# Performance work log

Hardware: AMD Instinct MI355X
Metric: run time of the kernel (lower is better)

## Reference

```python
import jax, jax.numpy as jnp
import numpy as np

D_MODEL = 2048
NUM_HEADS = 16
HEAD_DIM = D_MODEL // NUM_HEADS


def setup_inputs() -> dict:
    key = jax.random.key(0)
    ks = jax.random.split(key, 9)
    B, S, D = 2, 2048, D_MODEL
    scale = 1.0 / np.sqrt(D)
    x = jax.random.normal(ks[0], (B, S, D), dtype=jnp.float32)
    # torch nn.Linear weights are [out, in]; y = x @ W.T + b
    wq = jax.random.normal(ks[1], (D, D), dtype=jnp.float32) * scale
    wk = jax.random.normal(ks[2], (D, D), dtype=jnp.float32) * scale
    wv = jax.random.normal(ks[3], (D, D), dtype=jnp.float32) * scale
    wo = jax.random.normal(ks[4], (D, D), dtype=jnp.float32) * scale
    bq = jax.random.normal(ks[5], (D,), dtype=jnp.float32) * scale
    bk = jax.random.normal(ks[6], (D,), dtype=jnp.float32) * scale
    bv = jax.random.normal(ks[7], (D,), dtype=jnp.float32) * scale
    bo = jax.random.normal(ks[8], (D,), dtype=jnp.float32) * scale
    return {"x": x, "wq": wq, "bq": bq, "wk": wk, "bk": bk,
            "wv": wv, "bv": bv, "wo": wo, "bo": bo}


def reference(x, wq, bq, wk, bk, wv, bv, wo, bo):
    B, S, D = x.shape
    H, Dh = NUM_HEADS, HEAD_DIM
    # projections (torch Linear: x @ W.T + b), reshape to [B, H, S, Dh]
    q = (x @ wq.T + bq).reshape(B, S, H, Dh).transpose(0, 2, 1, 3)
    k = (x @ wk.T + bk).reshape(B, S, H, Dh).transpose(0, 2, 1, 3)
    v = (x @ wv.T + bv).reshape(B, S, H, Dh).transpose(0, 2, 1, 3)
    scores = jnp.einsum("bhqd,bhkd->bhqk", q, k) / jnp.sqrt(jnp.float32(Dh))
    attn = jax.nn.softmax(scores, axis=-1)
    out = jnp.einsum("bhqk,bhkd->bhqd", attn, v)  # [B, H, S, Dh]
    out = out.transpose(0, 2, 1, 3).reshape(B, S, D)
    return out @ wo.T + bo
```

## Files before the change

kernel.cpp:

```cpp
#include <hip/hip_runtime.h>

#define DEV __device__ __forceinline__

typedef __attribute__((ext_vector_type(8))) short bf16x8;
typedef __attribute__((ext_vector_type(4))) float f32x4;

constexpr int D_MODEL = 2048;
constexpr int NHEAD = 16;
constexpr int DH = 128;
constexpr int SS = 2048;
constexpr int KK = 2048;

DEV unsigned short f2bf(float f) {
  unsigned int u = __builtin_bit_cast(unsigned int, f);
  u = (u + 0x7fff + ((u >> 16) & 1)) >> 16;
  return (unsigned short)u;
}

DEV void async16(const void* g, void* l) {
  __builtin_amdgcn_global_load_lds(
      (const __attribute__((address_space(1))) unsigned int*)g,
      (__attribute__((address_space(3))) unsigned int*)l, 16, 0, 0);
}

DEV f32x4 mfma16(bf16x8 a, bf16x8 b, f32x4 c) {
  return __builtin_amdgcn_mfma_f32_16x16x32_bf16(a, b, c, 0, 0, 0);
}

__global__ __launch_bounds__(256) void cast_all(
    const float* __restrict__ x, const float* __restrict__ wq,
    const float* __restrict__ wk, const float* __restrict__ wv,
    const float* __restrict__ wo, unsigned short* __restrict__ xb,
    unsigned short* __restrict__ wb) {
  long i4 = ((long)blockIdx.x * 256 + threadIdx.x) * 4;
  const float* src;
  unsigned short* dst;
  long off;
  if (i4 < 8388608) {
    src = x; dst = xb; off = i4;
  } else {
    long j = i4 - 8388608;
    int seg = (int)(j >> 22);
    off = j & 4194303;
    src = (seg == 0) ? wq : (seg == 1) ? wk : (seg == 2) ? wv : wo;
    dst = wb + ((long)seg << 22);
  }
  float4 v = *(const float4*)(src + off);
  ushort4 u;
  u.x = f2bf(v.x); u.y = f2bf(v.y); u.z = f2bf(v.z); u.w = f2bf(v.w);
  *(ushort4*)(dst + off) = u;
}

template <int MODE>
__global__ __launch_bounds__(256, 2) void gemm_bt(
    const unsigned short* __restrict__ A, const unsigned short* __restrict__ W,
    const float* __restrict__ b0, const float* __restrict__ b1,
    const float* __restrict__ b2, unsigned short* __restrict__ oq,
    unsigned short* __restrict__ ok, unsigned short* __restrict__ ov,
    float* __restrict__ of) {
  __shared__ unsigned short lA[128 * 32];
  __shared__ unsigned short lB[128 * 32];
  const int t = threadIdx.x;
  const int lane = t & 63, wid = t >> 6;
  const int m0 = blockIdx.y * 128, n0 = blockIdx.x * 128;
  const int srow = t >> 2, scol = (t & 3) * 8;
  const unsigned short* ga = A + (long)(m0 + srow) * KK + scol;
  const unsigned short* gw = W + (long)(n0 + srow) * KK + scol;
  const int i16 = lane & 15, g4 = lane >> 4;
  const int wr = wid >> 1, wc = wid & 1;
  f32x4 acc[4][4] = {};
  for (int k0 = 0; k0 < KK; k0 += 32) {
    async16(ga + k0, &lA[wid * 512]);
    async16(ga + 64 * KK + k0, &lA[2048 + wid * 512]);
    async16(gw + k0, &lB[wid * 512]);
    async16(gw + 64 * KK + k0, &lB[2048 + wid * 512]);
    __syncthreads();
    bf16x8 af[4], bfr[4];
#pragma unroll
    for (int i = 0; i < 4; i++)
      af[i] = *(const bf16x8*)&lA[(wr * 64 + i * 16 + i16) * 32 + g4 * 8];
#pragma unroll
    for (int j = 0; j < 4; j++)
      bfr[j] = *(const bf16x8*)&lB[(wc * 64 + j * 16 + i16) * 32 + g4 * 8];
#pragma unroll
    for (int i = 0; i < 4; i++)
#pragma unroll
      for (int j = 0; j < 4; j++) acc[i][j] = mfma16(af[i], bfr[j], acc[i][j]);
    __syncthreads();
  }
#pragma unroll
  for (int i = 0; i < 4; i++) {
#pragma unroll
    for (int j = 0; j < 4; j++) {
      const int ng = n0 + wc * 64 + j * 16 + i16;
#pragma unroll
      for (int r = 0; r < 4; r++) {
        const int mg = m0 + wr * 64 + i * 16 + g4 * 4 + r;
        float v = acc[i][j][r];
        if (MODE == 1) {
          v += b0[ng];
          of[(long)mg * D_MODEL + ng] = v;
        } else {
          const int seg = ng >> 11, n = ng & 2047;
          const int h = n >> 7, d = n & 127;
          const int b_ = mg >> 11, s_ = mg & 2047;
          const long bh = b_ * NHEAD + h;
          if (seg == 0) {
            v = (v + b0[n]) * 0.08838834764831845f;
            oq[(bh * SS + s_) * DH + d] = f2bf(v);
          } else if (seg == 1) {
            v += b1[n];
            ok[(bh * SS + s_) * DH + d] = f2bf(v);
          } else {
            v += b2[n];
            ov[(bh * DH + d) * SS + s_] = f2bf(v);
          }
        }
      }
    }
  }
}

__global__ __launch_bounds__(256, 2) void attn_fwd(
    const unsigned short* __restrict__ Q, const unsigned short* __restrict__ Kb,
    const unsigned short* __restrict__ Vt, unsigned short* __restrict__ Ob) {
  __shared__ unsigned short lK[2][64 * 128];
  __shared__ unsigned short lV[2][128 * 64];
  __shared__ unsigned short lP[4][16 * 64];
  const int t = threadIdx.x, lane = t & 63, wid = t >> 6;
  const int i16 = lane & 15, g4 = lane >> 4;
  const int qt = blockIdx.x, bh = blockIdx.y;
  bf16x8 qa[2][4];
#pragma unroll
  for (int qi = 0; qi < 2; qi++) {
    const long qrow = (long)bh * SS + qt * 128 + wid * 32 + qi * 16 + i16;
#pragma unroll
    for (int ks = 0; ks < 4; ks++)
      qa[qi][ks] = *(const bf16x8*)&Q[qrow * DH + ks * 32 + g4 * 8];
  }
  f32x4 o[2][8] = {};
  float mrow[2][4] = {{-1e30f, -1e30f, -1e30f, -1e30f},
                      {-1e30f, -1e30f, -1e30f, -1e30f}};
  float lrow[2][4] = {};
  const char* kbase = (const char*)(Kb + (long)bh * SS * DH);
  const char* vbase = (const char*)(Vt + (long)bh * DH * SS);

  auto STAGE = [&](int buf, int kv0) {
#pragma unroll
    for (int r = 0; r < 4; r++) {
      const int o_ = r * 4096 + t * 16;
      const int okk = o_ ^ (((o_ >> 8) & 7) << 4);
      async16(kbase + (long)kv0 * 256 + okk,
              (char*)lK + buf * 16384 + r * 4096 + wid * 1024);
      const int vrow = o_ >> 7;
      const int inr = (o_ ^ ((vrow & 7) << 4)) & 127;
      async16(vbase + (long)vrow * (SS * 2) + kv0 * 2 + inr,
              (char*)lV + buf * 16384 + r * 4096 + wid * 1024);
    }
  };

  STAGE(0, 0);
  asm volatile("s_waitcnt vmcnt(0)");
  __syncthreads();
  int cur = 0;
  for (int it = 0; it < SS / 64; ++it) {
    if (it + 1 < SS / 64) STAGE(cur ^ 1, (it + 1) * 64);
    const char* kb = (const char*)lK + cur * 16384;
    const char* vb = (const char*)lV + cur * 16384;
    f32x4 s4[2][4] = {};
    __builtin_amdgcn_s_setprio(1);
#pragma unroll
    for (int kc = 0; kc < 4; kc++) {
      const int row = kc * 16 + i16;
#pragma unroll
      for (int ks = 0; ks < 4; ks++) {
        const int lb = row * 256 + ((ks * 64 + g4 * 16) ^ ((row & 7) << 4));
        bf16x8 kf = *(const bf16x8*)(kb + lb);
        s4[0][kc] = mfma16(qa[0][ks], kf, s4[0][kc]);
        s4[1][kc] = mfma16(qa[1][ks], kf, s4[1][kc]);
      }
    }
    __builtin_amdgcn_s_setprio(0);
    float fac[2][4];
#pragma unroll
    for (int qi = 0; qi < 2; qi++) {
#pragma unroll
      for (int r = 0; r < 4; r++) {
        float mx = fmaxf(fmaxf(s4[qi][0][r], s4[qi][1][r]),
                         fmaxf(s4[qi][2][r], s4[qi][3][r]));
        mx = fmaxf(mx, __shfl_xor(mx, 1));
        mx = fmaxf(mx, __shfl_xor(mx, 2));
        mx = fmaxf(mx, __shfl_xor(mx, 4));
        mx = fmaxf(mx, __shfl_xor(mx, 8));
        const float mnew = fmaxf(mrow[qi][r], mx);
        fac[qi][r] = __expf(mrow[qi][r] - mnew);
        mrow[qi][r] = mnew;
#pragma unroll
        for (int kc = 0; kc < 4; kc++)
          s4[qi][kc][r] = __expf(s4[qi][kc][r] - mnew);
        float su = s4[qi][0][r] + s4[qi][1][r] + s4[qi][2][r] + s4[qi][3][r];
        su += __shfl_xor(su, 1);
        su += __shfl_xor(su, 2);
        su += __shfl_xor(su, 4);
        su += __shfl_xor(su, 8);
        lrow[qi][r] = lrow[qi][r] * fac[qi][r] + su;
      }
    }
    bf16x8 pa[2][2];
#pragma unroll
    for (int qi = 0; qi < 2; qi++) {
#pragma unroll
      for (int r = 0; r < 4; r++) {
        const int prow = g4 * 4 + r;
        const int swz = (prow & 7) << 4;
#pragma unroll
        for (int kc = 0; kc < 4; kc++) {
          const int col = kc * 16 + i16;
          *(unsigned short*)((char*)&lP[wid][0] + prow * 128 +
                             ((col * 2) ^ swz)) = f2bf(s4[qi][kc][r]);
        }
      }
#pragma unroll
      for (int ks = 0; ks < 2; ks++) {
        const int lb = i16 * 128 + ((ks * 64 + g4 * 16) ^ ((i16 & 7) << 4));
        pa[qi][ks] = *(const bf16x8*)((const char*)&lP[wid][0] + lb);
      }
    }
#pragma unroll
    for (int qi = 0; qi < 2; qi++)
#pragma unroll
      for (int df = 0; df < 8; df++)
#pragma unroll
        for (int r = 0; r < 4; r++) o[qi][df][r] *= fac[qi][r];
    __builtin_amdgcn_s_setprio(1);
#pragma unroll
    for (int df = 0; df < 8; df++) {
#pragma unroll
      for (int ks = 0; ks < 2; ks++) {
        const int row = df * 16 + i16;
        const int lb = row * 128 + ((ks * 64 + g4 * 16) ^ ((row & 7) << 4));
        bf16x8 vf = *(const bf16x8*)(vb + lb);
        o[0][df] = mfma16(pa[0][ks], vf, o[0][df]);
        o[1][df] = mfma16(pa[1][ks], vf, o[1][df]);
      }
    }
    __builtin_amdgcn_s_setprio(0);
    asm volatile("s_waitcnt vmcnt(0)");
    __syncthreads();
    cur ^= 1;
  }
  const int b_ = bh >> 4, h = bh & 15;
#pragma unroll
  for (int qi = 0; qi < 2; qi++) {
#pragma unroll
    for (int df = 0; df < 8; df++) {
#pragma unroll
      for (int r = 0; r < 4; r++) {
        const float v = o[qi][df][r] / lrow[qi][r];
        const long mg =
            (long)b_ * SS + qt * 128 + wid * 32 + qi * 16 + g4 * 4 + r;
        Ob[mg * D_MODEL + h * DH + df * 16 + i16] = f2bf(v);
      }
    }
  }
}

extern "C" void kernel_launch(void* const* d_in, const int* in_sizes, int n_in,
                              void* d_out, int out_size, void* d_ws,
                              size_t ws_size, hipStream_t stream) {
  const float* x = (const float*)d_in[0];
  const float* wq = (const float*)d_in[1];
  const float* bq = (const float*)d_in[2];
  const float* wk = (const float*)d_in[3];
  const float* bk = (const float*)d_in[4];
  const float* wv = (const float*)d_in[5];
  const float* bv = (const float*)d_in[6];
  const float* wo = (const float*)d_in[7];
  const float* bo = (const float*)d_in[8];
  char* ws = (char*)d_ws;
  unsigned short* xb = (unsigned short*)(ws);
  unsigned short* wb = (unsigned short*)(ws + (16l << 20));
  unsigned short* wob = (unsigned short*)(ws + (40l << 20));
  unsigned short* Qb = (unsigned short*)(ws + (48l << 20));
  unsigned short* Kbf = (unsigned short*)(ws + (64l << 20));
  unsigned short* Vtb = (unsigned short*)(ws + (80l << 20));
  unsigned short* Atb = (unsigned short*)(ws);

  cast_all<<<24576, 256, 0, stream>>>(x, wq, wk, wv, wo, xb, wb);
  gemm_bt<0><<<dim3(48, 32), 256, 0, stream>>>(xb, wb, bq, bk, bv, Qb, Kbf,
                                               Vtb, nullptr);
  attn_fwd<<<dim3(16, 32), 256, 0, stream>>>(Qb, Kbf, Vtb, Atb);
  gemm_bt<1><<<dim3(16, 32), 256, 0, stream>>>(
      Atb, wob, bo, nullptr, nullptr, nullptr, nullptr, nullptr,
      (float*)d_out);
}
```

Measured before the change: 470.4 us.

## Use exp2 softmax with lazy rescaling and MFMA-computed row sums in attention

Folds log2(e) into the Q scaling so the softmax can use the raw v_exp_f32 (exp2) instruction directly. Output rescaling is skipped unless some row's running max grows by more than 8 (in log2 units), checked wave-uniformly with __all. Row sums are computed with an extra MFMA against a vector of bf16 ones instead of shuffle reductions, and the final divide becomes a reciprocal multiply. This removes per-tile shuffles, exps and rescale multiplies. In exchange it allows unnormalized values up to 2^8 and sums the bf16-rounded probabilities, which changes numerics slightly.

```diff
diff --git a/kernel.cpp b/kernel.cpp
--- a/kernel.cpp
+++ b/kernel.cpp
@@ -25,6 +25,12 @@
 
 DEV f32x4 mfma16(bf16x8 a, bf16x8 b, f32x4 c) {
   return __builtin_amdgcn_mfma_f32_16x16x32_bf16(a, b, c, 0, 0, 0);
+}
+
+DEV float exp2f_raw(float x) {
+  float y;
+  asm("v_exp_f32 %0, %1" : "=v"(y) : "v"(x));
+  return y;
 }
 
 __global__ __launch_bounds__(256) void cast_all(
@@ -106,7 +112,7 @@
           const int b_ = mg >> 11, s_ = mg & 2047;
           const long bh = b_ * NHEAD + h;
           if (seg == 0) {
-            v = (v + b0[n]) * 0.08838834764831845f;
+            v = (v + b0[n]) * (0.08838834764831845f * 1.4426950408889634f);
             oq[(bh * SS + s_) * DH + d] = f2bf(v);
           } else if (seg == 1) {
             v += b1[n];
@@ -138,10 +144,13 @@
     for (int ks = 0; ks < 4; ks++)
       qa[qi][ks] = *(const bf16x8*)&Q[qrow * DH + ks * 32 + g4 * 8];
   }
+  bf16x8 vones;
+#pragma unroll
+  for (int j = 0; j < 8; j++) vones[j] = (short)0x3F80;
   f32x4 o[2][8] = {};
+  f32x4 ol[2] = {};
   float mrow[2][4] = {{-1e30f, -1e30f, -1e30f, -1e30f},
                       {-1e30f, -1e30f, -1e30f, -1e30f}};
-  float lrow[2][4] = {};
   const char* kbase = (const char*)(Kb + (long)bh * SS * DH);
   const char* vbase = (const char*)(Vt + (long)bh * DH * SS);
 
@@ -181,30 +190,39 @@
       }
     }
     __builtin_amdgcn_s_setprio(0);
-    float fac[2][4];
 #pragma unroll
     for (int qi = 0; qi < 2; qi++) {
+      float mx[4];
 #pragma unroll
       for (int r = 0; r < 4; r++) {
-        float mx = fmaxf(fmaxf(s4[qi][0][r], s4[qi][1][r]),
+        float m_ = fmaxf(fmaxf(s4[qi][0][r], s4[qi][1][r]),
                          fmaxf(s4[qi][2][r], s4[qi][3][r]));
-        mx = fmaxf(mx, __shfl_xor(mx, 1));
-        mx = fmaxf(mx, __shfl_xor(mx, 2));
-        mx = fmaxf(mx, __shfl_xor(mx, 4));
-        mx = fmaxf(mx, __shfl_xor(mx, 8));
-        const float mnew = fmaxf(mrow[qi][r], mx);
-        fac[qi][r] = __expf(mrow[qi][r] - mnew);
-        mrow[qi][r] = mnew;
-#pragma unroll
-        for (int kc = 0; kc < 4; kc++)
-          s4[qi][kc][r] = __expf(s4[qi][kc][r] - mnew);
-        float su = s4[qi][0][r] + s4[qi][1][r] + s4[qi][2][r] + s4[qi][3][r];
-        su += __shfl_xor(su, 1);
-        su += __shfl_xor(su, 2);
-        su += __shfl_xor(su, 4);
-        su += __shfl_xor(su, 8);
-        lrow[qi][r] = lrow[qi][r] * fac[qi][r] + su;
-      }
+        m_ = fmaxf(m_, __shfl_xor(m_, 1));
+        m_ = fmaxf(m_, __shfl_xor(m_, 2));
+        m_ = fmaxf(m_, __shfl_xor(m_, 4));
+        m_ = fmaxf(m_, __shfl_xor(m_, 8));
+        mx[r] = m_;
+      }
+      const int ok = (mx[0] <= mrow[qi][0] + 8.f) &
+                     (mx[1] <= mrow[qi][1] + 8.f) &
+                     (mx[2] <= mrow[qi][2] + 8.f) &
+                     (mx[3] <= mrow[qi][3] + 8.f);
+      if (!__all(ok)) {
+#pragma unroll
+        for (int r = 0; r < 4; r++) {
+          const float mnew = fmaxf(mrow[qi][r], mx[r]);
+          const float fac = exp2f_raw(mrow[qi][r] - mnew);
+          mrow[qi][r] = mnew;
+          ol[qi][r] *= fac;
+#pragma unroll
+          for (int df = 0; df < 8; df++) o[qi][df][r] *= fac;
+        }
+      }
+#pragma unroll
+      for (int kc = 0; kc < 4; kc++)
+#pragma unroll
+        for (int r = 0; r < 4; r++)
+          s4[qi][kc][r] = exp2f_raw(s4[qi][kc][r] - mrow[qi][r]);
     }
     bf16x8 pa[2][2];
 #pragma unroll
@@ -226,13 +244,12 @@
         pa[qi][ks] = *(const bf16x8*)((const char*)&lP[wid][0] + lb);
       }
     }
-#pragma unroll
-    for (int qi = 0; qi < 2; qi++)
-#pragma unroll
-      for (int df = 0; df < 8; df++)
-#pragma unroll
-        for (int r = 0; r < 4; r++) o[qi][df][r] *= fac[qi][r];
     __builtin_amdgcn_s_setprio(1);
+#pragma unroll
+    for (int ks = 0; ks < 2; ks++) {
+      ol[0] = mfma16(pa[0][ks], vones, ol[0]);
+      ol[1] = mfma16(pa[1][ks], vones, ol[1]);
+    }
 #pragma unroll
     for (int df = 0; df < 8; df++) {
 #pragma unroll
@@ -252,11 +269,14 @@
   const int b_ = bh >> 4, h = bh & 15;
 #pragma unroll
   for (int qi = 0; qi < 2; qi++) {
+    float inv[4];
+#pragma unroll
+    for (int r = 0; r < 4; r++) inv[r] = __builtin_amdgcn_rcpf(ol[qi][r]);
 #pragma unroll
     for (int df = 0; df < 8; df++) {
 #pragma unroll
       for (int r = 0; r < 4; r++) {
-        const float v = o[qi][df][r] / lrow[qi][r];
+        const float v = o[qi][df][r] * inv[r];
         const long mg =
             (long)b_ * SS + qt * 128 + wid * 32 + qi * 16 + g4 * 4 + r;
         Ob[mg * D_MODEL + h * DH + df * 16 + i16] = f2bf(v);
```

Result: faster. 456.8 us (-2.9%).
